# Kernel tuning notes

Measured on AMD Instinct MI355X. Metric: run time of the kernel, lower is better.

Reference implementation:

```python
import jax, jax.numpy as jnp
import numpy as np

B, T, D, H, V = 4096, 193, 50, 50, 11


def setup_inputs() -> dict:
    key = jax.random.key(0)
    ks = jax.random.split(key, 7)
    s = 1.0 / np.sqrt(H)
    return {
        "x": jax.random.normal(ks[0], (B, T, D), dtype=jnp.float32),
        "W_ih": jax.random.uniform(ks[1], (4 * H, D), jnp.float32, -s, s),
        "W_hh": jax.random.uniform(ks[2], (4 * H, H), jnp.float32, -s, s),
        "b_ih": jax.random.uniform(ks[3], (4 * H,), jnp.float32, -s, s),
        "b_hh": jax.random.uniform(ks[4], (4 * H,), jnp.float32, -s, s),
        "fc_w": jax.random.uniform(ks[5], (V, H), jnp.float32, -s, s),
        "fc_b": jax.random.uniform(ks[6], (V,), jnp.float32, -s, s),
    }


def _lstm_last_h(x, W_ih, W_hh, b_ih, b_hh):
    # Precompute input projections for all timesteps: [T, B, 4H]
    xp = jnp.einsum("btd,gd->tbg", x, W_ih) + (b_ih + b_hh)
    h0 = jnp.zeros((x.shape[0], H), x.dtype)
    c0 = jnp.zeros((x.shape[0], H), x.dtype)

    def step(carry, xt):
        h, c = carry
        gates = xt + h @ W_hh.T  # [B, 4H]
        i, f, g, o = jnp.split(gates, 4, axis=-1)  # PyTorch gate order i,f,g,o
        i = jax.nn.sigmoid(i)
        f = jax.nn.sigmoid(f)
        g = jnp.tanh(g)
        o = jax.nn.sigmoid(o)
        c = f * c + i * g
        h = o * jnp.tanh(c)
        return (h, c), None

    (h_last, _), _ = jax.lax.scan(step, (h0, c0), xp)
    return h_last


def reference(x, W_ih, W_hh, b_ih, b_hh, fc_w, fc_b):
    h = _lstm_last_h(x, W_ih, W_hh, b_ih, b_hh)  # [B, H]
    logits = jax.nn.relu(h) @ fc_w.T + fc_b       # [B, V]
    return jax.nn.log_softmax(logits, axis=-1)
```

## Files before the change

kernel.cpp:

```cpp
#include <hip/hip_runtime.h>
#include <math.h>

#define B_   4096
#define T_   193
#define D_   50
#define H_   50
#define V_   11
#define BT   16
#define NBLK (B_ / BT)
#define CH   32
#define NCH  ((T_ + CH - 1) / CH)
#define NTHREADS 832
#define NP   ((CH * 128 + NTHREADS - 1) / NTHREADS)

typedef __bf16 bf16x8 __attribute__((ext_vector_type(8)));
typedef float  f32x4  __attribute__((ext_vector_type(4)));

__device__ __forceinline__ float sigf(float v) { return 1.0f / (1.0f + __expf(-v)); }
__device__ __forceinline__ float thf(float v)  { return 2.0f / (1.0f + __expf(-2.0f * v)) - 1.0f; }

__device__ __forceinline__ void lgkm_barrier() {
    asm volatile("s_waitcnt lgkmcnt(0)\n\ts_barrier" ::: "memory");
}

__global__ __launch_bounds__(NTHREADS) void lstm_mfma_kernel(
    const float* __restrict__ x,
    const float* __restrict__ W_ih,
    const float* __restrict__ W_hh,
    const float* __restrict__ b_ih,
    const float* __restrict__ b_hh,
    const float* __restrict__ fc_w,
    const float* __restrict__ fc_b,
    float* __restrict__ out)
{
    __shared__ __align__(16) unsigned short xs[2 * CH * 2 * 64 * 8];
    __shared__ __align__(16) unsigned short hb[2 * 2 * 64 * 8];
    __shared__ float hfin[BT * 53];
    __shared__ float lgts[BT][V_];

    const int tid  = threadIdx.x;
    const int wid  = tid >> 6;
    const int lane = tid & 63;
    const int n    = lane & 15;
    const int kg   = lane >> 4;
    const int row0 = blockIdx.x * BT;
    const int tile = wid;

    if (tid < 256) {
        int4 z; z.x = 0; z.y = 0; z.z = 0; z.w = 0;
        reinterpret_cast<int4*>(hb)[tid] = z;
    }
    if (tid < 32) {
        hb[((tid >> 4) * 2 + 1) * 512 + (48 + (tid & 15)) * 8 + 7] = 0x3F80;
    }

    bf16x8 wf[4];
    {
        #pragma unroll
        for (int s = 0; s < 4; ++s) {
            float tv[8];
            #pragma unroll
            for (int j = 0; j < 8; ++j) tv[j] = 0.0f;
            const int gp = 16 * tile + n;
            const int q  = gp & 3;
            const int ju = gp >> 2;
            if (ju < 50) {
                const int row = q * 50 + ju;
                #pragma unroll
                for (int j = 0; j < 8; ++j) {
                    const int k = s * 32 + kg * 8 + j;
                    float v = 0.0f;
                    if (k < 50)                  v = W_ih[row * 50 + k];
                    else if (k >= 64 && k < 114) v = W_hh[row * 50 + (k - 64)];
                    else if (k == 127)           v = b_ih[row] + b_hh[row];
                    tv[j] = v;
                }
            }
            bf16x8 w;
            #pragma unroll
            for (int j = 0; j < 8; ++j) w[j] = (__bf16)tv[j];
            wf[s] = w;
        }
    }

    const int u_   = 4 * tile + kg;
    const int hoff = (u_ >> 5) * 512 + ((((u_ & 31) >> 3) << 4) | n) * 8 + (u_ & 7);

    float2 P[NP][4];

    auto loadChunk = [&](int c) {
        const int t0 = c * CH;
        const int L  = (T_ - t0 < CH) ? (T_ - t0) : CH;
        const int nfrag = L * 128;
        #pragma unroll
        for (int i = 0; i < NP; ++i) {
            const int fi = tid + i * NTHREADS;
            if (fi < nfrag) {
                const int tc  = fi >> 7;
                const int rem = fi & 127;
                const int s   = rem >> 6;
                const int l   = rem & 63;
                const int nn  = l & 15;
                const int kk  = l >> 4;
                const float* base = x + ((size_t)(row0 + nn) * T_ + (t0 + tc)) * D_;
                #pragma unroll
                for (int j = 0; j < 4; ++j) {
                    int col = 32 * s + kk * 8 + 2 * j;
                    if (col > 48) col = 48;
                    P[i][j] = *reinterpret_cast<const float2*>(base + col);
                }
            }
        }
    };
    auto writeChunk = [&](int c, int b) {
        const int t0 = c * CH;
        const int L  = (T_ - t0 < CH) ? (T_ - t0) : CH;
        const int nfrag = L * 128;
        #pragma unroll
        for (int i = 0; i < NP; ++i) {
            const int fi = tid + i * NTHREADS;
            if (fi < nfrag) {
                bf16x8 w;
                #pragma unroll
                for (int j = 0; j < 4; ++j) {
                    w[2 * j]     = (__bf16)P[i][j].x;
                    w[2 * j + 1] = (__bf16)P[i][j].y;
                }
                reinterpret_cast<int4*>(xs)[b * (CH * 128) + fi] =
                    __builtin_bit_cast(int4, w);
            }
        }
    };

    loadChunk(0);
    writeChunk(0, 0);
    __syncthreads();
    loadChunk(1);

    float cst = 0.0f;
    float hlast = 0.0f;
    int cur = 0;
    const int4* xsv = reinterpret_cast<const int4*>(xs);

    for (int c = 0; c < NCH; ++c) {
        const int t0 = c * CH;
        const int L  = (T_ - t0 < CH) ? (T_ - t0) : CH;
        const int b  = c & 1;

        f32x4 ax;
        {
            const bf16x8 bx0 = __builtin_bit_cast(bf16x8, xsv[b * (CH * 128) + lane]);
            const bf16x8 bx1 = __builtin_bit_cast(bf16x8, xsv[b * (CH * 128) + 64 + lane]);
            f32x4 z = {0.0f, 0.0f, 0.0f, 0.0f};
            z  = __builtin_amdgcn_mfma_f32_16x16x32_bf16(wf[0], bx0, z, 0, 0, 0);
            ax = __builtin_amdgcn_mfma_f32_16x16x32_bf16(wf[1], bx1, z, 0, 0, 0);
        }

        for (int tc = 0; tc < L; ++tc) {
            const int4* hbv = reinterpret_cast<const int4*>(hb) + cur * 128;
            const bf16x8 bh0 = __builtin_bit_cast(bf16x8, hbv[lane]);
            const bf16x8 bh1 = __builtin_bit_cast(bf16x8, hbv[64 + lane]);
            f32x4 a = __builtin_amdgcn_mfma_f32_16x16x32_bf16(wf[2], bh0, ax, 0, 0, 0);
            a = __builtin_amdgcn_mfma_f32_16x16x32_bf16(wf[3], bh1, a, 0, 0, 0);

            const float ii = sigf(a[0]);
            const float ff = sigf(a[1]);
            const float g2 = thf(a[2]);
            const float oo = sigf(a[3]);
            cst = ff * cst + ii * g2;
            const float h = oo * thf(cst);
            hlast = h;
            hb[(cur ^ 1) * 1024 + hoff] =
                __builtin_bit_cast(unsigned short, (__bf16)h);

            if (tc + 1 < L) {
                const bf16x8 nx0 = __builtin_bit_cast(
                    bf16x8, xsv[b * (CH * 128) + (tc + 1) * 128 + lane]);
                const bf16x8 nx1 = __builtin_bit_cast(
                    bf16x8, xsv[b * (CH * 128) + (tc + 1) * 128 + 64 + lane]);
                f32x4 z = {0.0f, 0.0f, 0.0f, 0.0f};
                z  = __builtin_amdgcn_mfma_f32_16x16x32_bf16(wf[0], nx0, z, 0, 0, 0);
                ax = __builtin_amdgcn_mfma_f32_16x16x32_bf16(wf[1], nx1, z, 0, 0, 0);
            }

            if (tc == L - 1) {
                if (c + 1 < NCH) writeChunk(c + 1, b ^ 1);
                if (c + 2 < NCH) loadChunk(c + 2);
            }

            lgkm_barrier();
            cur ^= 1;
        }
    }

    hfin[n * 53 + u_] = hlast;
    __syncthreads();

    if (tid < BT * V_) {
        const int bn = tid / V_;
        const int v  = tid % V_;
        float a = fc_b[v];
        #pragma unroll
        for (int j = 0; j < 50; ++j) {
            float hj = hfin[bn * 53 + j];
            hj = hj > 0.0f ? hj : 0.0f;
            a = fmaf(hj, fc_w[v * 50 + j], a);
        }
        lgts[bn][v] = a;
    }
    __syncthreads();
    if (tid < BT * V_) {
        const int bn = tid / V_;
        const int v  = tid % V_;
        float m = -1e30f;
        #pragma unroll
        for (int u = 0; u < V_; ++u) m = fmaxf(m, lgts[bn][u]);
        float s = 0.0f;
        #pragma unroll
        for (int u = 0; u < V_; ++u) s += __expf(lgts[bn][u] - m);
        out[(size_t)(row0 + bn) * V_ + v] = lgts[bn][v] - m - __logf(s);
    }
}

extern "C" void kernel_launch(void* const* d_in, const int* in_sizes, int n_in,
                              void* d_out, int out_size, void* d_ws, size_t ws_size,
                              hipStream_t stream) {
    const float* x    = (const float*)d_in[0];
    const float* W_ih = (const float*)d_in[1];
    const float* W_hh = (const float*)d_in[2];
    const float* b_ih = (const float*)d_in[3];
    const float* b_hh = (const float*)d_in[4];
    const float* fc_w = (const float*)d_in[5];
    const float* fc_b = (const float*)d_in[6];
    float* out = (float*)d_out;

    lstm_mfma_kernel<<<NBLK, NTHREADS, 0, stream>>>(
        x, W_ih, W_hh, b_ih, b_hh, fc_w, fc_b, out);
}
```

Measured before the change: 180.2 us.

## Split bf16 hi/lo weights and hidden state, two tiles per wave

Splits W_ih, W_hh and the hidden state into bf16 high and low parts and adds extra MFMAs to approximate fp32 accuracy. Each wave now handles two gate tiles (448 threads, 2 blocks per CU), and the chunk size drops to 16. The time loop is unrolled so the last-timestep tail is peeled out. This roughly triples the MFMA work on the serial recurrence path and doubles the hidden-state LDS traffic, in exchange for better accuracy and higher occupancy.

```diff
diff --git a/kernel.cpp b/kernel.cpp
--- a/kernel.cpp
+++ b/kernel.cpp
@@ -8,10 +8,10 @@
 #define V_   11
 #define BT   16
 #define NBLK (B_ / BT)
-#define CH   32
+#define CH   16
 #define NCH  ((T_ + CH - 1) / CH)
-#define NTHREADS 832
-#define NP   ((CH * 128 + NTHREADS - 1) / NTHREADS)
+#define NTHREADS 448
+#define NP   5
 
 typedef __bf16 bf16x8 __attribute__((ext_vector_type(8)));
 typedef float  f32x4  __attribute__((ext_vector_type(4)));
@@ -23,7 +23,7 @@
     asm volatile("s_waitcnt lgkmcnt(0)\n\ts_barrier" ::: "memory");
 }
 
-__global__ __launch_bounds__(NTHREADS) void lstm_mfma_kernel(
+__global__ __launch_bounds__(NTHREADS, 2) void lstm_mfma_kernel(
     const float* __restrict__ x,
     const float* __restrict__ W_ih,
     const float* __restrict__ W_hh,
@@ -34,7 +34,7 @@
     float* __restrict__ out)
 {
     __shared__ __align__(16) unsigned short xs[2 * CH * 2 * 64 * 8];
-    __shared__ __align__(16) unsigned short hb[2 * 2 * 64 * 8];
+    __shared__ __align__(16) unsigned short hb[2 * 4 * 64 * 8];
     __shared__ float hfin[BT * 53];
     __shared__ float lgts[BT][V_];
 
@@ -44,47 +44,54 @@
     const int n    = lane & 15;
     const int kg   = lane >> 4;
     const int row0 = blockIdx.x * BT;
-    const int tile = wid;
-
-    if (tid < 256) {
+    const int tA   = 2 * wid;
+    const int tB   = 2 * wid + 1;
+
+    {
         int4 z; z.x = 0; z.y = 0; z.z = 0; z.w = 0;
-        reinterpret_cast<int4*>(hb)[tid] = z;
-    }
+        #pragma unroll
+        for (int i = tid; i < 512; i += NTHREADS)
+            reinterpret_cast<int4*>(hb)[i] = z;
+    }
+    __syncthreads();
     if (tid < 32) {
-        hb[((tid >> 4) * 2 + 1) * 512 + (48 + (tid & 15)) * 8 + 7] = 0x3F80;
-    }
-
-    bf16x8 wf[4];
-    {
-        #pragma unroll
-        for (int s = 0; s < 4; ++s) {
-            float tv[8];
+        hb[(tid >> 4) * 2048 + 512 + (48 + (tid & 15)) * 8 + 7] = 0x3F80;
+    }
+
+    bf16x8 wxhA[2], wxlA[2], whhA[2], whlA[2];
+    bf16x8 wxhB[2], wxlB[2], whhB[2], whlB[2];
+    #pragma unroll
+    for (int ti = 0; ti < 2; ++ti) {
+        const int gp = 16 * (ti == 0 ? tA : tB) + n;
+        const int q  = gp & 3;
+        const int ju = gp >> 2;
+        const bool real = (ju < 50);
+        const int row = real ? (q * 50 + ju) : 0;
+        #pragma unroll
+        for (int s = 0; s < 2; ++s) {
+            bf16x8 xh, xl, hh, hl;
             #pragma unroll
-            for (int j = 0; j < 8; ++j) tv[j] = 0.0f;
-            const int gp = 16 * tile + n;
-            const int q  = gp & 3;
-            const int ju = gp >> 2;
-            if (ju < 50) {
-                const int row = q * 50 + ju;
-                #pragma unroll
-                for (int j = 0; j < 8; ++j) {
-                    const int k = s * 32 + kg * 8 + j;
-                    float v = 0.0f;
-                    if (k < 50)                  v = W_ih[row * 50 + k];
-                    else if (k >= 64 && k < 114) v = W_hh[row * 50 + (k - 64)];
-                    else if (k == 127)           v = b_ih[row] + b_hh[row];
-                    tv[j] = v;
+            for (int j = 0; j < 8; ++j) {
+                const int k = s * 32 + kg * 8 + j;
+                float vx = 0.0f, vh = 0.0f;
+                if (real) {
+                    if (k < 50) { vx = W_ih[row * 50 + k]; vh = W_hh[row * 50 + k]; }
+                    if (k == 63) vh = b_ih[row] + b_hh[row];
                 }
+                const __bf16 xhi = (__bf16)vx;
+                const __bf16 hhi = (__bf16)vh;
+                xh[j] = xhi; xl[j] = (__bf16)(vx - (float)xhi);
+                hh[j] = hhi; hl[j] = (__bf16)(vh - (float)hhi);
             }
-            bf16x8 w;
-            #pragma unroll
-            for (int j = 0; j < 8; ++j) w[j] = (__bf16)tv[j];
-            wf[s] = w;
-        }
-    }
-
-    const int u_   = 4 * tile + kg;
-    const int hoff = (u_ >> 5) * 512 + ((((u_ & 31) >> 3) << 4) | n) * 8 + (u_ & 7);
+            if (ti == 0) { wxhA[s] = xh; wxlA[s] = xl; whhA[s] = hh; whlA[s] = hl; }
+            else         { wxhB[s] = xh; wxlB[s] = xl; whhB[s] = hh; whlB[s] = hl; }
+        }
+    }
+
+    const int uA = 4 * tA + kg;
+    const int uB = 4 * tB + kg;
+    const int hoffA = (uA >> 5) * 512 + ((((uA & 31) >> 3) << 4) | n) * 8 + (uA & 7);
+    const int hoffB = (uB >> 5) * 512 + ((((uB & 31) >> 3) << 4) | n) * 8 + (uB & 7);
 
     float2 P[NP][4];
 
@@ -137,63 +144,125 @@
     __syncthreads();
     loadChunk(1);
 
-    float cst = 0.0f;
-    float hlast = 0.0f;
-    int cur = 0;
+    float cstA = 0.0f, cstB = 0.0f;
+    float hlastA = 0.0f, hlastB = 0.0f;
+    const f32x4 zz = {0.0f, 0.0f, 0.0f, 0.0f};
+    f32x4 axA, axB;
     const int4* xsv = reinterpret_cast<const int4*>(xs);
-
-    for (int c = 0; c < NCH; ++c) {
-        const int t0 = c * CH;
-        const int L  = (T_ - t0 < CH) ? (T_ - t0) : CH;
-        const int b  = c & 1;
-
-        f32x4 ax;
+    const int4* hbv = reinterpret_cast<const int4*>(hb);
+
+#define XPROJ(X0, X1)                                                         \
+    {                                                                         \
+        axA = __builtin_amdgcn_mfma_f32_16x16x32_bf16(wxhA[0], (X0), zz, 0, 0, 0);  \
+        axA = __builtin_amdgcn_mfma_f32_16x16x32_bf16(wxhA[1], (X1), axA, 0, 0, 0); \
+        axA = __builtin_amdgcn_mfma_f32_16x16x32_bf16(wxlA[0], (X0), axA, 0, 0, 0); \
+        axA = __builtin_amdgcn_mfma_f32_16x16x32_bf16(wxlA[1], (X1), axA, 0, 0, 0); \
+        axB = __builtin_amdgcn_mfma_f32_16x16x32_bf16(wxhB[0], (X0), zz, 0, 0, 0);  \
+        axB = __builtin_amdgcn_mfma_f32_16x16x32_bf16(wxhB[1], (X1), axB, 0, 0, 0); \
+        axB = __builtin_amdgcn_mfma_f32_16x16x32_bf16(wxlB[0], (X0), axB, 0, 0, 0); \
+        axB = __builtin_amdgcn_mfma_f32_16x16x32_bf16(wxlB[1], (X1), axB, 0, 0, 0); \
+    }
+
+#define STEP(CUR, TC, LAST)                                                   \
+    {                                                                         \
+        const int4* hc = hbv + (CUR) * 256;                                   \
+        const bf16x8 bh0 = __builtin_bit_cast(bf16x8, hc[lane]);              \
+        const bf16x8 bh1 = __builtin_bit_cast(bf16x8, hc[64 + lane]);         \
+        const bf16x8 bl0 = __builtin_bit_cast(bf16x8, hc[128 + lane]);        \
+        const bf16x8 bl1 = __builtin_bit_cast(bf16x8, hc[192 + lane]);        \
+        f32x4 aA = __builtin_amdgcn_mfma_f32_16x16x32_bf16(whhA[0], bh0, axA, 0, 0, 0); \
+        aA = __builtin_amdgcn_mfma_f32_16x16x32_bf16(whhA[1], bh1, aA, 0, 0, 0);        \
+        aA = __builtin_amdgcn_mfma_f32_16x16x32_bf16(whhA[0], bl0, aA, 0, 0, 0);        \
+        aA = __builtin_amdgcn_mfma_f32_16x16x32_bf16(whhA[1], bl1, aA, 0, 0, 0);        \
+        aA = __builtin_amdgcn_mfma_f32_16x16x32_bf16(whlA[0], bh0, aA, 0, 0, 0);        \
+        aA = __builtin_amdgcn_mfma_f32_16x16x32_bf16(whlA[1], bh1, aA, 0, 0, 0);        \
+        f32x4 aB = __builtin_amdgcn_mfma_f32_16x16x32_bf16(whhB[0], bh0, axB, 0, 0, 0); \
+        aB = __builtin_amdgcn_mfma_f32_16x16x32_bf16(whhB[1], bh1, aB, 0, 0, 0);        \
+        aB = __builtin_amdgcn_mfma_f32_16x16x32_bf16(whhB[0], bl0, aB, 0, 0, 0);        \
+        aB = __builtin_amdgcn_mfma_f32_16x16x32_bf16(whhB[1], bl1, aB, 0, 0, 0);        \
+        aB = __builtin_amdgcn_mfma_f32_16x16x32_bf16(whlB[0], bh0, aB, 0, 0, 0);        \
+        aB = __builtin_amdgcn_mfma_f32_16x16x32_bf16(whlB[1], bh1, aB, 0, 0, 0);        \
+        const float iiA = sigf(aA[0]);                                        \
+        const float ffA = sigf(aA[1]);                                        \
+        const float g2A = thf(aA[2]);                                         \
+        const float ooA = sigf(aA[3]);                                        \
+        cstA = fmaf(ffA, cstA, iiA * g2A);                                    \
+        const float hA = ooA * thf(cstA);                                     \
+        const float iiB = sigf(aB[0]);                                        \
+        const float ffB = sigf(aB[1]);                                        \
+        const float g2B = thf(aB[2]);                                         \
+        const float ooB = sigf(aB[3]);                                        \
+        cstB = fmaf(ffB, cstB, iiB * g2B);                                    \
+        const float hB = ooB * thf(cstB);                                     \
+        const __bf16 hAhi = (__bf16)hA;                                       \
+        const __bf16 hBhi = (__bf16)hB;                                       \
+        const __bf16 hAlo = (__bf16)(hA - (float)hAhi);                       \
+        const __bf16 hBlo = (__bf16)(hB - (float)hBhi);                       \
+        unsigned short* hw = hb + ((CUR) ^ 1) * 2048;                         \
+        hw[hoffA]        = __builtin_bit_cast(unsigned short, hAhi);          \
+        hw[hoffB]        = __builtin_bit_cast(unsigned short, hBhi);          \
+        hw[1024 + hoffA] = __builtin_bit_cast(unsigned short, hAlo);          \
+        hw[1024 + hoffB] = __builtin_bit_cast(unsigned short, hBlo);          \
+        if (!(LAST)) {                                                        \
+            const bf16x8 nx0 = __builtin_bit_cast(                            \
+                bf16x8, xb[((TC) + 1) * 128 + lane]);                         \
+            const bf16x8 nx1 = __builtin_bit_cast(                            \
+                bf16x8, xb[((TC) + 1) * 128 + 64 + lane]);                    \
+            XPROJ(nx0, nx1);                                                  \
+        } else {                                                              \
+            writeChunk(c + 1, bb ^ 1);                                        \
+            if (c + 2 < NCH) loadChunk(c + 2);                                \
+        }                                                                     \
+        lgkm_barrier();                                                       \
+    }
+
+    for (int c = 0; c < NCH - 1; ++c) {
+        const int bb = c & 1;
+        const int4* xb = xsv + bb * (CH * 128);
+
         {
-            const bf16x8 bx0 = __builtin_bit_cast(bf16x8, xsv[b * (CH * 128) + lane]);
-            const bf16x8 bx1 = __builtin_bit_cast(bf16x8, xsv[b * (CH * 128) + 64 + lane]);
-            f32x4 z = {0.0f, 0.0f, 0.0f, 0.0f};
-            z  = __builtin_amdgcn_mfma_f32_16x16x32_bf16(wf[0], bx0, z, 0, 0, 0);
-            ax = __builtin_amdgcn_mfma_f32_16x16x32_bf16(wf[1], bx1, z, 0, 0, 0);
-        }
-
-        for (int tc = 0; tc < L; ++tc) {
-            const int4* hbv = reinterpret_cast<const int4*>(hb) + cur * 128;
-            const bf16x8 bh0 = __builtin_bit_cast(bf16x8, hbv[lane]);
-            const bf16x8 bh1 = __builtin_bit_cast(bf16x8, hbv[64 + lane]);
-            f32x4 a = __builtin_amdgcn_mfma_f32_16x16x32_bf16(wf[2], bh0, ax, 0, 0, 0);
-            a = __builtin_amdgcn_mfma_f32_16x16x32_bf16(wf[3], bh1, a, 0, 0, 0);
-
-            const float ii = sigf(a[0]);
-            const float ff = sigf(a[1]);
-            const float g2 = thf(a[2]);
-            const float oo = sigf(a[3]);
-            cst = ff * cst + ii * g2;
-            const float h = oo * thf(cst);
-            hlast = h;
-            hb[(cur ^ 1) * 1024 + hoff] =
-                __builtin_bit_cast(unsigned short, (__bf16)h);
-
-            if (tc + 1 < L) {
-                const bf16x8 nx0 = __builtin_bit_cast(
-                    bf16x8, xsv[b * (CH * 128) + (tc + 1) * 128 + lane]);
-                const bf16x8 nx1 = __builtin_bit_cast(
-                    bf16x8, xsv[b * (CH * 128) + (tc + 1) * 128 + 64 + lane]);
-                f32x4 z = {0.0f, 0.0f, 0.0f, 0.0f};
-                z  = __builtin_amdgcn_mfma_f32_16x16x32_bf16(wf[0], nx0, z, 0, 0, 0);
-                ax = __builtin_amdgcn_mfma_f32_16x16x32_bf16(wf[1], nx1, z, 0, 0, 0);
-            }
-
-            if (tc == L - 1) {
-                if (c + 1 < NCH) writeChunk(c + 1, b ^ 1);
-                if (c + 2 < NCH) loadChunk(c + 2);
-            }
-
-            lgkm_barrier();
-            cur ^= 1;
-        }
-    }
-
-    hfin[n * 53 + u_] = hlast;
+            const bf16x8 x0 = __builtin_bit_cast(bf16x8, xb[lane]);
+            const bf16x8 x1 = __builtin_bit_cast(bf16x8, xb[64 + lane]);
+            XPROJ(x0, x1);
+        }
+        #pragma unroll
+        for (int p = 0; p < 8; ++p) {
+            STEP(0, 2 * p, 0);
+            STEP(1, 2 * p + 1, (2 * p + 1 == CH - 1));
+        }
+    }
+
+    {
+        const int4* xb = xsv;
+        const bf16x8 x0 = __builtin_bit_cast(bf16x8, xb[lane]);
+        const bf16x8 x1 = __builtin_bit_cast(bf16x8, xb[64 + lane]);
+        XPROJ(x0, x1);
+
+        const bf16x8 bh0 = __builtin_bit_cast(bf16x8, hbv[lane]);
+        const bf16x8 bh1 = __builtin_bit_cast(bf16x8, hbv[64 + lane]);
+        const bf16x8 bl0 = __builtin_bit_cast(bf16x8, hbv[128 + lane]);
+        const bf16x8 bl1 = __builtin_bit_cast(bf16x8, hbv[192 + lane]);
+        f32x4 aA = __builtin_amdgcn_mfma_f32_16x16x32_bf16(whhA[0], bh0, axA, 0, 0, 0);
+        aA = __builtin_amdgcn_mfma_f32_16x16x32_bf16(whhA[1], bh1, aA, 0, 0, 0);
+        aA = __builtin_amdgcn_mfma_f32_16x16x32_bf16(whhA[0], bl0, aA, 0, 0, 0);
+        aA = __builtin_amdgcn_mfma_f32_16x16x32_bf16(whhA[1], bl1, aA, 0, 0, 0);
+        aA = __builtin_amdgcn_mfma_f32_16x16x32_bf16(whlA[0], bh0, aA, 0, 0, 0);
+        aA = __builtin_amdgcn_mfma_f32_16x16x32_bf16(whlA[1], bh1, aA, 0, 0, 0);
+        f32x4 aB = __builtin_amdgcn_mfma_f32_16x16x32_bf16(whhB[0], bh0, axB, 0, 0, 0);
+        aB = __builtin_amdgcn_mfma_f32_16x16x32_bf16(whhB[1], bh1, aB, 0, 0, 0);
+        aB = __builtin_amdgcn_mfma_f32_16x16x32_bf16(whhB[0], bl0, aB, 0, 0, 0);
+        aB = __builtin_amdgcn_mfma_f32_16x16x32_bf16(whhB[1], bl1, aB, 0, 0, 0);
+        aB = __builtin_amdgcn_mfma_f32_16x16x32_bf16(whlB[0], bh0, aB, 0, 0, 0);
+        aB = __builtin_amdgcn_mfma_f32_16x16x32_bf16(whlB[1], bh1, aB, 0, 0, 0);
+
+        cstA = fmaf(sigf(aA[1]), cstA, sigf(aA[0]) * thf(aA[2]));
+        hlastA = sigf(aA[3]) * thf(cstA);
+        cstB = fmaf(sigf(aB[1]), cstB, sigf(aB[0]) * thf(aB[2]));
+        hlastB = sigf(aB[3]) * thf(cstB);
+    }
+
+    if (uA < 50) hfin[n * 53 + uA] = hlastA;
+    if (uB < 50) hfin[n * 53 + uB] = hlastB;
     __syncthreads();
 
     if (tid < BT * V_) {
```

Result: slower. 214.3 us (+18.9%).
